# Kernel tuning notes

Hardware: AMD Instinct MI355X
Metric: run time of the kernel (lower is better)

## Reference

```python
import jax, jax.numpy as jnp
import numpy as np

E4M3_AMAX = 216.0   # HPU constant: 240 * 0.9
FP8_MAX = 240.0     # saturation bound used by cast_to_fp8 on HPU e4m3


def _quant_fp8(x, scale):
    """Dynamic per-tensor fp8 quantize: scale, saturate, round-to-fp8, back to f32."""
    y = jnp.clip(x * scale, -FP8_MAX, FP8_MAX)
    return y.astype(jnp.float8_e4m3fn).astype(jnp.float32)


def setup_inputs() -> dict:
    key = jax.random.key(0)
    k1, k2, k3 = jax.random.split(key, 3)
    inp = jax.random.normal(k1, (4, 4096, 4096), dtype=jnp.float32)
    weight = jax.random.normal(k2, (4096, 4096), dtype=jnp.float32) * 0.02
    bias = jax.random.normal(k3, (4096,), dtype=jnp.float32)
    return {"inp": inp, "weight": weight, "bias": bias}


def reference(inp, weight, bias):
    # weight quantization (done once at init in the torch module; same math)
    w_scale = E4M3_AMAX / jnp.max(jnp.abs(weight))
    w8 = _quant_fp8(weight, w_scale)                      # [out, in]
    # dynamic activation quantization (per forward call)
    i_scale = E4M3_AMAX / jnp.max(jnp.abs(inp))
    x2d = inp.reshape(-1, weight.shape[1])                # [tokens, in]
    x8 = _quant_fp8(x2d, i_scale)
    # fp8_gemm_v2: dequantize by the inverse scales in the epilogue, add bias
    out = (x8 @ w8.T) * (1.0 / i_scale) * (1.0 / w_scale) + bias  # [tokens, out]
    return out.reshape(*inp.shape[:-1], out.shape[-1])
```

## Files before the change

kernel.cpp:

```cpp
#include <hip/hip_runtime.h>

typedef unsigned char u8;
typedef unsigned int u32;
using f32x4 = __attribute__((ext_vector_type(4))) float;

#define E4M3_AMAX 216.0f
#define FP8_MAXV 240.0f

#define BM 128
#define BN 128
#define BK 64

#define GLD_LDS16(g, l) \
    __builtin_amdgcn_global_load_lds((const __attribute__((address_space(1))) void*)(g), \
                                     (__attribute__((address_space(3))) void*)(l), 16, 0, 0)

__global__ void maxabs_kernel(const float* __restrict__ x, long n4, u32* __restrict__ out) {
    long stride = (long)gridDim.x * blockDim.x;
    long i = (long)blockIdx.x * blockDim.x + threadIdx.x;
    u32 m = 0;
    const float4* x4 = (const float4*)x;
    for (long j = i; j < n4; j += stride) {
        float4 v = x4[j];
        u32 a = __float_as_uint(fabsf(v.x));
        u32 b = __float_as_uint(fabsf(v.y));
        u32 c = __float_as_uint(fabsf(v.z));
        u32 d = __float_as_uint(fabsf(v.w));
        m = a > m ? a : m;
        m = b > m ? b : m;
        m = c > m ? c : m;
        m = d > m ? d : m;
    }
    #pragma unroll
    for (int off = 32; off > 0; off >>= 1) {
        u32 o = (u32)__shfl_down((unsigned int)m, (unsigned int)off, 64);
        m = o > m ? o : m;
    }
    __shared__ u32 sm[8];
    int wave = threadIdx.x >> 6, lane = threadIdx.x & 63;
    if (lane == 0) sm[wave] = m;
    __syncthreads();
    if (threadIdx.x == 0) {
        u32 r = sm[0];
        int nw = blockDim.x >> 6;
        for (int w = 1; w < nw; ++w) r = sm[w] > r ? sm[w] : r;
        atomicMax(out, r);
    }
}

__global__ void quant_kernel(const float* __restrict__ x, u8* __restrict__ y, long n4,
                             const u32* __restrict__ maxbits, int idx) {
    float mx = __uint_as_float(maxbits[idx]);
    float scale = E4M3_AMAX / mx;
    long stride = (long)gridDim.x * blockDim.x;
    long i = (long)blockIdx.x * blockDim.x + threadIdx.x;
    const float4* x4 = (const float4*)x;
    int* y4 = (int*)y;
    for (long j = i; j < n4; j += stride) {
        float4 v = x4[j];
        float a = fminf(fmaxf(v.x * scale, -FP8_MAXV), FP8_MAXV);
        float b = fminf(fmaxf(v.y * scale, -FP8_MAXV), FP8_MAXV);
        float c = fminf(fmaxf(v.z * scale, -FP8_MAXV), FP8_MAXV);
        float d = fminf(fmaxf(v.w * scale, -FP8_MAXV), FP8_MAXV);
        int p = 0;
        p = __builtin_amdgcn_cvt_pk_fp8_f32(a, b, p, false);
        p = __builtin_amdgcn_cvt_pk_fp8_f32(c, d, p, true);
        y4[j] = p;
    }
}

__global__ __launch_bounds__(256) void gemm_fp8_kernel(
    const u8* __restrict__ A,
    const u8* __restrict__ B,
    const float* __restrict__ bias,
    const u32* __restrict__ scales,
    float* __restrict__ C, int M, int N, int K)
{
    __shared__ u8 As[BM * BK];
    __shared__ u8 Bs[BN * BK];

    const int tid = threadIdx.x;
    const int wave = tid >> 6;
    const int lane = tid & 63;
    const int fr = lane & 15;
    const int quad = lane >> 4;

    const int bm = blockIdx.y * BM;
    const int bn = blockIdx.x * BN;
    const int wm = (wave >> 1) * 64;
    const int wn = (wave & 1) * 64;

    f32x4 acc[4][4] = {};

    const int srow = 16 * wave + (lane >> 2);
    const int swzs = (lane >> 3) & 3;
    const int scol = ((lane & 3) ^ swzs) * 16;
    const u8* gA = A + (size_t)(bm + srow) * K + scol;
    const u8* gB = B + (size_t)(bn + srow) * K + scol;
    u8* lA = As + wave * 1024;
    u8* lB = Bs + wave * 1024;

    const int swzr = (fr >> 1) & 3;

    for (int k0 = 0; k0 < K; k0 += BK) {
        GLD_LDS16(gA,              lA);
        GLD_LDS16(gA + (size_t)64 * K, lA + 4096);
        GLD_LDS16(gB,              lB);
        GLD_LDS16(gB + (size_t)64 * K, lB + 4096);
        gA += BK;
        gB += BK;
        __syncthreads();

        #pragma unroll
        for (int ks = 0; ks < 2; ++ks) {
            const int colx = (ks * 32 + quad * 8) ^ (swzr << 4);
            long a[4], b[4];
            #pragma unroll
            for (int i = 0; i < 4; ++i) {
                a[i] = *(const long*)(As + (wm + i * 16 + fr) * BK + colx);
                b[i] = *(const long*)(Bs + (wn + i * 16 + fr) * BK + colx);
            }
            #pragma unroll
            for (int i = 0; i < 4; ++i)
                #pragma unroll
                for (int j = 0; j < 4; ++j)
                    acc[i][j] = __builtin_amdgcn_mfma_f32_16x16x32_fp8_fp8(a[i], b[j], acc[i][j], 0, 0, 0);
        }
        __syncthreads();
    }

    const float mi = __uint_as_float(scales[0]);
    const float mw = __uint_as_float(scales[1]);
    const float i_scale = E4M3_AMAX / mi;
    const float w_scale = E4M3_AMAX / mw;
    const float deq = (1.0f / i_scale) * (1.0f / w_scale);

    #pragma unroll
    for (int i = 0; i < 4; ++i) {
        const int row0 = bm + wm + i * 16 + quad * 4;
        #pragma unroll
        for (int j = 0; j < 4; ++j) {
            const int col = bn + wn + j * 16 + fr;
            const float bv = bias[col];
            #pragma unroll
            for (int rg = 0; rg < 4; ++rg) {
                C[(size_t)(row0 + rg) * N + col] = acc[i][j][rg] * deq + bv;
            }
        }
    }
}

extern "C" void kernel_launch(void* const* d_in, const int* in_sizes, int n_in,
                              void* d_out, int out_size, void* d_ws, size_t ws_size,
                              hipStream_t stream) {
    const float* inp    = (const float*)d_in[0];
    const float* weight = (const float*)d_in[1];
    const float* bias   = (const float*)d_in[2];
    float* out = (float*)d_out;

    const int N = in_sizes[2];
    const int K = in_sizes[1] / N;
    const long icount = in_sizes[0];
    const int M = (int)(icount / K);
    const long wcount = (long)N * K;

    u32* scales = (u32*)d_ws;
    u8* x8 = (u8*)d_ws + 256;
    u8* w8 = x8 + (size_t)M * K;

    hipMemsetAsync(d_ws, 0, 16, stream);

    maxabs_kernel<<<2048, 256, 0, stream>>>(inp, icount / 4, scales + 0);
    maxabs_kernel<<<1024, 256, 0, stream>>>(weight, wcount / 4, scales + 1);

    quant_kernel<<<4096, 256, 0, stream>>>(inp, x8, icount / 4, scales, 0);
    quant_kernel<<<2048, 256, 0, stream>>>(weight, w8, wcount / 4, scales, 1);

    dim3 grid(N / BN, M / BM);
    gemm_fp8_kernel<<<grid, 256, 0, stream>>>(x8, w8, bias, scales, out, M, N, K);
}
```

Measured before the change: 992.1 us.

## Double-buffer GEMM LDS tiles, swizzle workgroups, and merge max/quant kernels

The GEMM main loop now uses two LDS buffers, so the next K-tile's global-to-LDS load is issued before computing the current one, overlapping memory with MFMA. Workgroup IDs are remapped across 8 groups, presumably to spread tiles over XCDs for better L2 reuse. The separate maxabs and quant launches for input and weight are merged into single launches, and quant now writes 16 bytes per thread. This doubles LDS use per workgroup, which may lower occupancy. The unrolled loop assumes K is a multiple of 2*BK.

New measurement: 887.2 us. 10.6% less time.

```diff
diff --git a/kernel.cpp b/kernel.cpp
--- a/kernel.cpp
+++ b/kernel.cpp
@@ -15,21 +15,31 @@
     __builtin_amdgcn_global_load_lds((const __attribute__((address_space(1))) void*)(g), \
                                      (__attribute__((address_space(3))) void*)(l), 16, 0, 0)
 
-__global__ void maxabs_kernel(const float* __restrict__ x, long n4, u32* __restrict__ out) {
-    long stride = (long)gridDim.x * blockDim.x;
-    long i = (long)blockIdx.x * blockDim.x + threadIdx.x;
+__global__ void maxabs2_kernel(const float* __restrict__ a, long na4, u32* __restrict__ outa,
+                               const float* __restrict__ b, long nb4, u32* __restrict__ outb,
+                               int blocksA) {
+    const float4* x4;
+    long n4;
+    u32* out;
+    long bid, nb;
+    if ((int)blockIdx.x < blocksA) {
+        x4 = (const float4*)a; n4 = na4; out = outa; bid = blockIdx.x; nb = blocksA;
+    } else {
+        x4 = (const float4*)b; n4 = nb4; out = outb; bid = blockIdx.x - blocksA; nb = gridDim.x - blocksA;
+    }
+    long stride = nb * blockDim.x;
+    long i = bid * blockDim.x + threadIdx.x;
     u32 m = 0;
-    const float4* x4 = (const float4*)x;
     for (long j = i; j < n4; j += stride) {
         float4 v = x4[j];
-        u32 a = __float_as_uint(fabsf(v.x));
-        u32 b = __float_as_uint(fabsf(v.y));
-        u32 c = __float_as_uint(fabsf(v.z));
-        u32 d = __float_as_uint(fabsf(v.w));
-        m = a > m ? a : m;
-        m = b > m ? b : m;
-        m = c > m ? c : m;
-        m = d > m ? d : m;
+        u32 pa = __float_as_uint(fabsf(v.x));
+        u32 pb = __float_as_uint(fabsf(v.y));
+        u32 pc = __float_as_uint(fabsf(v.z));
+        u32 pd = __float_as_uint(fabsf(v.w));
+        m = pa > m ? pa : m;
+        m = pb > m ? pb : m;
+        m = pc > m ? pc : m;
+        m = pd > m ? pd : m;
     }
     #pragma unroll
     for (int off = 32; off > 0; off >>= 1) {
@@ -48,24 +58,64 @@
     }
 }
 
-__global__ void quant_kernel(const float* __restrict__ x, u8* __restrict__ y, long n4,
-                             const u32* __restrict__ maxbits, int idx) {
-    float mx = __uint_as_float(maxbits[idx]);
+__global__ void quant2_kernel(const float* __restrict__ a, u8* __restrict__ ya, long na16,
+                              const float* __restrict__ b, u8* __restrict__ yb, long nb16,
+                              const u32* __restrict__ maxbits, int blocksA) {
+    const float4* x4;
+    int4* y4;
+    long n16, bid, nb;
+    float mx;
+    if ((int)blockIdx.x < blocksA) {
+        x4 = (const float4*)a; y4 = (int4*)ya; n16 = na16; bid = blockIdx.x; nb = blocksA;
+        mx = __uint_as_float(maxbits[0]);
+    } else {
+        x4 = (const float4*)b; y4 = (int4*)yb; n16 = nb16; bid = blockIdx.x - blocksA; nb = gridDim.x - blocksA;
+        mx = __uint_as_float(maxbits[1]);
+    }
     float scale = E4M3_AMAX / mx;
-    long stride = (long)gridDim.x * blockDim.x;
-    long i = (long)blockIdx.x * blockDim.x + threadIdx.x;
-    const float4* x4 = (const float4*)x;
-    int* y4 = (int*)y;
-    for (long j = i; j < n4; j += stride) {
-        float4 v = x4[j];
-        float a = fminf(fmaxf(v.x * scale, -FP8_MAXV), FP8_MAXV);
-        float b = fminf(fmaxf(v.y * scale, -FP8_MAXV), FP8_MAXV);
-        float c = fminf(fmaxf(v.z * scale, -FP8_MAXV), FP8_MAXV);
-        float d = fminf(fmaxf(v.w * scale, -FP8_MAXV), FP8_MAXV);
-        int p = 0;
-        p = __builtin_amdgcn_cvt_pk_fp8_f32(a, b, p, false);
-        p = __builtin_amdgcn_cvt_pk_fp8_f32(c, d, p, true);
-        y4[j] = p;
+    long stride = nb * blockDim.x;
+    long i = bid * blockDim.x + threadIdx.x;
+    for (long j = i; j < n16; j += stride) {
+        int4 p4;
+        #pragma unroll
+        for (int q = 0; q < 4; ++q) {
+            float4 v = x4[j * 4 + q];
+            float pa = fminf(fmaxf(v.x * scale, -FP8_MAXV), FP8_MAXV);
+            float pb = fminf(fmaxf(v.y * scale, -FP8_MAXV), FP8_MAXV);
+            float pc = fminf(fmaxf(v.z * scale, -FP8_MAXV), FP8_MAXV);
+            float pd = fminf(fmaxf(v.w * scale, -FP8_MAXV), FP8_MAXV);
+            int p = 0;
+            p = __builtin_amdgcn_cvt_pk_fp8_f32(pa, pb, p, false);
+            p = __builtin_amdgcn_cvt_pk_fp8_f32(pc, pd, p, true);
+            ((int*)&p4)[q] = p;
+        }
+        y4[j] = p4;
+    }
+}
+
+__device__ __forceinline__ void stage_tile(const u8* gA, const u8* gB, u8* lA, u8* lB, int K) {
+    GLD_LDS16(gA,                  lA);
+    GLD_LDS16(gA + (size_t)64 * K, lA + 4096);
+    GLD_LDS16(gB,                  lB);
+    GLD_LDS16(gB + (size_t)64 * K, lB + 4096);
+}
+
+__device__ __forceinline__ void compute_tile(const u8* Asb, const u8* Bsb, f32x4 acc[4][4],
+                                             int wm, int wn, int fr, int quad, int swzr) {
+    #pragma unroll
+    for (int ks = 0; ks < 2; ++ks) {
+        const int colx = (ks * 32 + quad * 8) ^ (swzr << 4);
+        long a[4], b[4];
+        #pragma unroll
+        for (int i = 0; i < 4; ++i) {
+            a[i] = *(const long*)(Asb + (wm + i * 16 + fr) * BK + colx);
+            b[i] = *(const long*)(Bsb + (wn + i * 16 + fr) * BK + colx);
+        }
+        #pragma unroll
+        for (int i = 0; i < 4; ++i)
+            #pragma unroll
+            for (int j = 0; j < 4; ++j)
+                acc[i][j] = __builtin_amdgcn_mfma_f32_16x16x32_fp8_fp8(a[i], b[j], acc[i][j], 0, 0, 0);
     }
 }
 
@@ -76,8 +126,7 @@
     const u32* __restrict__ scales,
     float* __restrict__ C, int M, int N, int K)
 {
-    __shared__ u8 As[BM * BK];
-    __shared__ u8 Bs[BN * BK];
+    __shared__ u8 smem[2][2 * BM * BK];
 
     const int tid = threadIdx.x;
     const int wave = tid >> 6;
@@ -85,8 +134,16 @@
     const int fr = lane & 15;
     const int quad = lane >> 4;
 
-    const int bm = blockIdx.y * BM;
-    const int bn = blockIdx.x * BN;
+    const int nwg = (int)(gridDim.x * gridDim.y);
+    int orig = (int)(blockIdx.y * gridDim.x + blockIdx.x);
+    int swz = orig;
+    if ((nwg & 7) == 0) {
+        const int cpx = nwg >> 3;
+        swz = (orig & 7) * cpx + (orig >> 3);
+    }
+    const int bm = (swz / (int)gridDim.x) * BM;
+    const int bn = (swz % (int)gridDim.x) * BN;
+
     const int wm = (wave >> 1) * 64;
     const int wn = (wave & 1) * 64;
 
@@ -97,36 +154,25 @@
     const int scol = ((lane & 3) ^ swzs) * 16;
     const u8* gA = A + (size_t)(bm + srow) * K + scol;
     const u8* gB = B + (size_t)(bn + srow) * K + scol;
-    u8* lA = As + wave * 1024;
-    u8* lB = Bs + wave * 1024;
+    const int lofs = wave * 1024;
+
+    u8* As0 = smem[0];            u8* Bs0 = smem[0] + BM * BK;
+    u8* As1 = smem[1];            u8* Bs1 = smem[1] + BM * BK;
 
     const int swzr = (fr >> 1) & 3;
 
-    for (int k0 = 0; k0 < K; k0 += BK) {
-        GLD_LDS16(gA,              lA);
-        GLD_LDS16(gA + (size_t)64 * K, lA + 4096);
-        GLD_LDS16(gB,              lB);
-        GLD_LDS16(gB + (size_t)64 * K, lB + 4096);
-        gA += BK;
-        gB += BK;
+    stage_tile(gA, gB, As0 + lofs, Bs0 + lofs, K);
+
+    for (int k0 = 0; k0 < K; k0 += 2 * BK) {
         __syncthreads();
-
-        #pragma unroll
-        for (int ks = 0; ks < 2; ++ks) {
-            const int colx = (ks * 32 + quad * 8) ^ (swzr << 4);
-            long a[4], b[4];
-            #pragma unroll
-            for (int i = 0; i < 4; ++i) {
-                a[i] = *(const long*)(As + (wm + i * 16 + fr) * BK + colx);
-                b[i] = *(const long*)(Bs + (wn + i * 16 + fr) * BK + colx);
-            }
-            #pragma unroll
-            for (int i = 0; i < 4; ++i)
-                #pragma unroll
-                for (int j = 0; j < 4; ++j)
-                    acc[i][j] = __builtin_amdgcn_mfma_f32_16x16x32_fp8_fp8(a[i], b[j], acc[i][j], 0, 0, 0);
-        }
+        if (k0 + BK < K)
+            stage_tile(gA + (k0 + BK), gB + (k0 + BK), As1 + lofs, Bs1 + lofs, K);
+        compute_tile(As0, Bs0, acc, wm, wn, fr, quad, swzr);
+
         __syncthreads();
+        if (k0 + 2 * BK < K)
+            stage_tile(gA + (k0 + 2 * BK), gB + (k0 + 2 * BK), As0 + lofs, Bs0 + lofs, K);
+        compute_tile(As1, Bs1, acc, wm, wn, fr, quad, swzr);
     }
 
     const float mi = __uint_as_float(scales[0]);
@@ -170,11 +216,10 @@
 
     hipMemsetAsync(d_ws, 0, 16, stream);
 
-    maxabs_kernel<<<2048, 256, 0, stream>>>(inp, icount / 4, scales + 0);
-    maxabs_kernel<<<1024, 256, 0, stream>>>(weight, wcount / 4, scales + 1);
-
-    quant_kernel<<<4096, 256, 0, stream>>>(inp, x8, icount / 4, scales, 0);
-    quant_kernel<<<2048, 256, 0, stream>>>(weight, w8, wcount / 4, scales, 1);
+    maxabs2_kernel<<<2560, 256, 0, stream>>>(inp, icount / 4, scales + 0,
+                                             weight, wcount / 4, scales + 1, 2048);
+    quant2_kernel<<<2560, 256, 0, stream>>>(inp, x8, icount / 16,
+                                            weight, w8, wcount / 16, scales, 2048);
 
     dim3 grid(N / BN, M / BM);
     gemm_fp8_kernel<<<grid, 256, 0, stream>>>(x8, w8, bias, scales, out, M, N, K);
```
